# Kernel tuning notes

Hardware: AMD Instinct MI355X
Metric: run time of the kernel (lower is better)

Reference implementation:

```python
import jax, jax.numpy as jnp
import numpy as np

NUM_QUBITS = 12
ENC_COPIES = 1
ANSATZ_COPIES = 2
BATCH = 1024
NUM_THETAS = NUM_QUBITS * (ANSATZ_COPIES + 1) * 2  # 72

_H = jnp.asarray(np.array([[1.0, 1.0], [1.0, -1.0]], np.complex64) / np.sqrt(2.0))


def _apply_1q(state, U, q):
    # state: [B, 2, 2, ..., 2] (n qubit axes); apply 2x2 unitary U on qubit q
    s = jnp.moveaxis(state, 1 + q, -1)
    s = jnp.einsum('...j,ij->...i', s, U)
    return jnp.moveaxis(s, -1, 1 + q)


def _apply_zpow(state, t, q):
    # cirq Z**t = diag(1, e^{i*pi*t}); t is scalar or per-batch [B]
    n = state.ndim - 1
    phase = jnp.exp(1j * jnp.pi * t).astype(jnp.complex64)
    factor = jnp.stack([jnp.ones_like(phase), phase], axis=-1)
    if factor.ndim == 2:  # batched exponent -> broadcast over other qubit axes
        factor = factor.reshape((factor.shape[0],) + (1,) * (n - 1) + (2,))
    s = jnp.moveaxis(state, 1 + q, -1)
    return jnp.moveaxis(s * factor, -1, 1 + q)


def _ypow_unitary(t):
    # cirq Y**t up to global phase e^{i*pi*t/2} (irrelevant for Z expectations)
    a = 0.5 * jnp.pi * t
    c, s = jnp.cos(a), jnp.sin(a)
    return jnp.stack([jnp.stack([c, -s]), jnp.stack([s, c])]).astype(jnp.complex64)


def _apply_cnot(state, c, t):
    s = jnp.moveaxis(state, (1 + c, 1 + t), (-2, -1))
    s = jnp.stack([s[..., 0, :], s[..., 1, ::-1]], axis=-2)
    return jnp.moveaxis(s, (-2, -1), (1 + c, 1 + t))


def _encoding_block(state, x):
    # FirstOrderPauliZEncoding: per copy, per qubit: H then Z**x_q
    for _ in range(ENC_COPIES):
        for q in range(NUM_QUBITS):
            state = _apply_1q(state, _H, q)
            state = _apply_zpow(state, x[:, q], q)
    return state


def _ansatz_block(state, th, with_cnot):
    # EfficientSU2 layer: Y**th[q,0], Z**th[q,1] per qubit, then CNOT chain
    for q in range(NUM_QUBITS):
        state = _apply_1q(state, _ypow_unitary(th[q, 0]), q)
        state = _apply_zpow(state, th[q, 1], q)
    if with_cnot:
        for q in range(NUM_QUBITS - 1):
            state = _apply_cnot(state, q, q + 1)
    return state


_enc = jax.checkpoint(_encoding_block)
_ans_cnot = jax.checkpoint(lambda st, th: _ansatz_block(st, th, True))
_ans_last = jax.checkpoint(lambda st, th: _ansatz_block(st, th, False))


def _circuit(inputs, thetas):
    b = inputs.shape[0]
    state = jnp.zeros((b, 2 ** NUM_QUBITS), jnp.complex64).at[:, 0].set(1.0)
    state = state.reshape((b,) + (2,) * NUM_QUBITS)
    state = _enc(state, inputs)
    th = thetas.reshape(ANSATZ_COPIES + 1, NUM_QUBITS, 2)
    for l in range(ANSATZ_COPIES + 1):
        state = (_ans_cnot if l < ANSATZ_COPIES else _ans_last)(state, th[l])
    # readouts: <Z_q> for each qubit
    probs = state.real ** 2 + state.imag ** 2
    exps = []
    for q in range(NUM_QUBITS):
        axes = tuple(a for a in range(1, NUM_QUBITS + 1) if a != 1 + q)
        p = probs.sum(axis=axes)  # [B, 2]
        exps.append(p[:, 0] - p[:, 1])
    return jnp.stack(exps, axis=-1)  # [B, NUM_QUBITS]


def setup_inputs() -> dict:
    key = jax.random.key(0)
    k1, k2 = jax.random.split(key)
    inputs = jax.random.uniform(k1, (BATCH, NUM_QUBITS), jnp.float32)
    thetas = jax.random.uniform(k2, (NUM_THETAS,), jnp.float32, minval=-1.0, maxval=1.0)
    return {"inputs": inputs, "thetas": thetas}


def reference(inputs, thetas):
    return _circuit(inputs, thetas)
```

## Files before the change

kernel.cpp:

```cpp
#include <hip/hip_runtime.h>


#define PI_F 3.14159265358979323846f
#define NR 32
#define PAD 66

__device__ __forceinline__ float2 cmul(float2 a, float2 b) {
    return make_float2(a.x*b.x - a.y*b.y, a.x*b.y + a.y*b.x);
}
__device__ __forceinline__ float2 cmulc(float2 a, float2 b) {
    return make_float2(a.x*b.x + a.y*b.y, a.y*b.x - a.x*b.y);
}

template<int RB>
__device__ __forceinline__ void ypow_reg(float2 (&a)[NR], float c, float s) {
    #pragma unroll
    for (int r0 = 0; r0 < NR; ++r0) {
        if ((r0 >> RB) & 1) continue;
        const int r1 = r0 | (1 << RB);
        float2 a0 = a[r0], a1 = a[r1];
        a[r0] = make_float2(c*a0.x - s*a1.x, c*a0.y - s*a1.y);
        a[r1] = make_float2(s*a0.x + c*a1.x, s*a0.y + c*a1.y);
    }
}

__device__ __forceinline__ void exchange_AB(float2 (&a)[NR], float2* buf,
                                            int w, int lane, float c6, float s6) {
    float2* wb = buf + w * (NR * PAD);
    __syncthreads();
    #pragma unroll
    for (int r = 0; r < NR; ++r)
        wb[r * PAD + (lane & 31) * 2 + (lane >> 5)] = a[r];
    __syncthreads();
    const int g = lane >> 1;
    const float k0 = (lane & 1) ? s6 : c6;
    const float k1 = (lane & 1) ? c6 : -s6;
    #pragma unroll
    for (int r = 0; r < NR; ++r) {
        float2 p0 = wb[g * PAD + r * 2];
        float2 p1 = wb[g * PAD + r * 2 + 1];
        a[r] = make_float2(k0*p0.x + k1*p1.x, k0*p0.y + k1*p1.y);
    }
}

__device__ __forceinline__ void exchange_BA(float2 (&a)[NR], float2* buf,
                                            int w, int lane, float c0, float s0) {
    __syncthreads();
    const int p6w = lane ^ (w << 5);
    #pragma unroll
    for (int r = 0; r < NR; ++r)
        buf[p6w * PAD + r * 2 + w] = a[r];
    __syncthreads();
    const float k0 = w ? s0 : c0;
    const float k1 = w ? c0 : -s0;
    #pragma unroll
    for (int rp = 0; rp < NR; ++rp) {
        const int ylow = (rp << 6) | lane;
        const int t = ylow ^ (ylow >> 1);
        const int base = (t >> 5) * PAD + (t & 31) * 2;
        float2 p0 = buf[base];
        float2 p1 = buf[base + 1];
        a[rp] = make_float2(k0*p0.x + k1*p1.x, k0*p0.y + k1*p1.y);
    }
}

__device__ __forceinline__ void ypow_block_regA(float2 (&a)[NR], const float* __restrict__ th) {
    { float s,c; __sincosf(0.5f*PI_F*th[2],  &s,&c); ypow_reg<4>(a,c,s); }
    { float s,c; __sincosf(0.5f*PI_F*th[4],  &s,&c); ypow_reg<3>(a,c,s); }
    { float s,c; __sincosf(0.5f*PI_F*th[6],  &s,&c); ypow_reg<2>(a,c,s); }
    { float s,c; __sincosf(0.5f*PI_F*th[8],  &s,&c); ypow_reg<1>(a,c,s); }
    { float s,c; __sincosf(0.5f*PI_F*th[10], &s,&c); ypow_reg<0>(a,c,s); }
}
__device__ __forceinline__ void ypow_block_regB(float2 (&a)[NR], const float* __restrict__ th) {
    { float s,c; __sincosf(0.5f*PI_F*th[14], &s,&c); ypow_reg<4>(a,c,s); }
    { float s,c; __sincosf(0.5f*PI_F*th[16], &s,&c); ypow_reg<3>(a,c,s); }
    { float s,c; __sincosf(0.5f*PI_F*th[18], &s,&c); ypow_reg<2>(a,c,s); }
    { float s,c; __sincosf(0.5f*PI_F*th[20], &s,&c); ypow_reg<1>(a,c,s); }
    { float s,c; __sincosf(0.5f*PI_F*th[22], &s,&c); ypow_reg<0>(a,c,s); }
}

__device__ __forceinline__ void fused_z_B(float2 (&a)[NR], int w, int lane,
                                          const float* __restrict__ th) {
    float alpha = w ? th[1] : 0.0f;
    #pragma unroll
    for (int k = 0; k < 6; ++k)
        alpha += ((lane >> k) & 1) ? th[2*(6-k)+1] : 0.0f;
    float2 zb; __sincosf(PI_F * alpha, &zb.y, &zb.x);
    float2 zq[5];
    #pragma unroll
    for (int j = 0; j < 5; ++j)
        __sincosf(PI_F * th[2*(11-j)+1], &zq[j].y, &zq[j].x);
    float2 cur = zb;
    a[0] = cmul(a[0], cur);
    #pragma unroll
    for (int k = 1; k < NR; ++k) {
        const int bit = __builtin_ctz(k);
        const int g = k ^ (k >> 1);
        cur = ((g >> bit) & 1) ? cmul(cur, zq[bit]) : cmulc(cur, zq[bit]);
        a[g] = cmul(a[g], cur);
    }
}

__global__ __launch_bounds__(128) void vqc_kernel(
    const float* __restrict__ inputs,
    const float* __restrict__ thetas,
    float* __restrict__ out)
{
    __shared__ __align__(16) float2 buf[64 * PAD];
    __shared__ float redBuf[24];

    const int b = blockIdx.x;
    const int tid = threadIdx.x;
    const int w = tid >> 6;
    const int lane = tid & 63;
    const float* x = inputs + b * 12;

    float2 a[NR];

    float phb = 0.0f;
    #pragma unroll
    for (int k = 0; k < 6; ++k)
        phb += ((lane >> k) & 1) ? x[11 - k] : 0.0f;
    float2 cisb; __sincosf(PI_F * phb, &cisb.y, &cisb.x);
    float2 E;    __sincosf(PI_F * x[0], &E.y, &E.x);
    float s0, c0; __sincosf(0.5f * PI_F * thetas[0], &s0, &c0);
    float2 Fw = w ? make_float2(s0 + c0 * E.x,  c0 * E.y)
                  : make_float2(c0 - s0 * E.x, -s0 * E.y);
    float2 g0 = cmul(Fw, cisb);
    g0.x *= 0.015625f; g0.y *= 0.015625f;
    float2 zr[5];
    #pragma unroll
    for (int j = 0; j < 5; ++j)
        __sincosf(PI_F * x[5 - j], &zr[j].y, &zr[j].x);
    {
        float2 cur = g0;
        a[0] = cur;
        #pragma unroll
        for (int k = 1; k < NR; ++k) {
            const int bit = __builtin_ctz(k);
            const int g = k ^ (k >> 1);
            cur = ((g >> bit) & 1) ? cmul(cur, zr[bit]) : cmulc(cur, zr[bit]);
            a[g] = cur;
        }
    }

    const float* th0 = thetas;
    const float* th1 = thetas + 24;
    const float* th2 = thetas + 48;

    ypow_block_regA(a, th0);
    { float s,c; __sincosf(0.5f*PI_F*th0[12], &s,&c); exchange_AB(a, buf, w, lane, c, s); }
    ypow_block_regB(a, th0);
    fused_z_B(a, w, lane, th0);
    { float s,c; __sincosf(0.5f*PI_F*th1[0],  &s,&c); exchange_BA(a, buf, w, lane, c, s); }

    ypow_block_regA(a, th1);
    { float s,c; __sincosf(0.5f*PI_F*th1[12], &s,&c); exchange_AB(a, buf, w, lane, c, s); }
    ypow_block_regB(a, th1);
    fused_z_B(a, w, lane, th1);
    { float s,c; __sincosf(0.5f*PI_F*th2[0],  &s,&c); exchange_BA(a, buf, w, lane, c, s); }

    ypow_block_regA(a, th2);
    { float s,c; __sincosf(0.5f*PI_F*th2[12], &s,&c); exchange_AB(a, buf, w, lane, c, s); }
    ypow_block_regB(a, th2);

    float totalP = 0.0f;
    float D[5] = {0, 0, 0, 0, 0};
    #pragma unroll
    for (int r = 0; r < NR; ++r) {
        const float p = a[r].x * a[r].x + a[r].y * a[r].y;
        totalP += p;
        #pragma unroll
        for (int j = 0; j < 5; ++j)
            D[j] += ((r >> j) & 1) ? -p : p;
    }
    #pragma unroll
    for (int q = 0; q < 12; ++q) {
        float v;
        if (q == 0)       v = w ? -totalP : totalP;
        else if (q <= 6)  v = ((lane >> (6 - q)) & 1) ? -totalP : totalP;
        else              v = D[11 - q];
        #pragma unroll
        for (int off = 32; off >= 1; off >>= 1)
            v += __shfl_xor(v, off, 64);
        if (lane == 0) redBuf[w * 12 + q] = v;
    }
    __syncthreads();
    if (tid < 12) out[b * 12 + tid] = redBuf[tid] + redBuf[12 + tid];
}

extern "C" void kernel_launch(void* const* d_in, const int* in_sizes, int n_in,
                              void* d_out, int out_size, void* d_ws, size_t ws_size,
                              hipStream_t stream) {
    const float* inputs = (const float*)d_in[0];
    const float* thetas = (const float*)d_in[1];
    float* out = (float*)d_out;
    vqc_kernel<<<dim3(1024), dim3(128), 0, stream>>>(inputs, thetas, out);
}
```

Baseline: 78.01 us.

## Split state across four wavefronts with 16 registers each and swizzled LDS exchanges

Each batch item now runs on 256 threads (four waves) holding 16 amplitudes per thread instead of 128 threads holding 32. Two qubits move from registers to the wave index, so the exchanges and the encoding, Z-phase and readout logic are rewritten to apply paired 2x2 rotations through XOR-swizzled 32 KB shared buffers read as float4. The exchange after the first ansatz layer drops its leading barrier and relies on an s_waitcnt instead. The goal is lower register pressure and more parallelism per item, at the cost of more shared memory per block and more LDS traffic per amplitude.

New measurement: 146.7 us. 1.88x slower.

```diff
diff --git a/kernel.cpp b/kernel.cpp
--- a/kernel.cpp
+++ b/kernel.cpp
@@ -2,8 +2,7 @@
 
 
 #define PI_F 3.14159265358979323846f
-#define NR 32
-#define PAD 66
+#define NR 16
 
 __device__ __forceinline__ float2 cmul(float2 a, float2 b) {
     return make_float2(a.x*b.x - a.y*b.y, a.x*b.y + a.y*b.x);
@@ -24,71 +23,88 @@
     }
 }
 
-__device__ __forceinline__ void exchange_AB(float2 (&a)[NR], float2* buf,
-                                            int w, int lane, float c6, float s6) {
-    float2* wb = buf + w * (NR * PAD);
-    __syncthreads();
-    #pragma unroll
-    for (int r = 0; r < NR; ++r)
-        wb[r * PAD + (lane & 31) * 2 + (lane >> 5)] = a[r];
-    __syncthreads();
-    const int g = lane >> 1;
-    const float k0 = (lane & 1) ? s6 : c6;
-    const float k1 = (lane & 1) ? c6 : -s6;
-    #pragma unroll
-    for (int r = 0; r < NR; ++r) {
-        float2 p0 = wb[g * PAD + r * 2];
-        float2 p1 = wb[g * PAD + r * 2 + 1];
-        a[r] = make_float2(k0*p0.x + k1*p1.x, k0*p0.y + k1*p1.y);
-    }
-}
-
-__device__ __forceinline__ void exchange_BA(float2 (&a)[NR], float2* buf,
-                                            int w, int lane, float c0, float s0) {
-    __syncthreads();
-    const int p6w = lane ^ (w << 5);
-    #pragma unroll
-    for (int r = 0; r < NR; ++r)
-        buf[p6w * PAD + r * 2 + w] = a[r];
-    __syncthreads();
-    const float k0 = w ? s0 : c0;
-    const float k1 = w ? c0 : -s0;
-    #pragma unroll
-    for (int rp = 0; rp < NR; ++rp) {
-        const int ylow = (rp << 6) | lane;
-        const int t = ylow ^ (ylow >> 1);
-        const int base = (t >> 5) * PAD + (t & 31) * 2;
-        float2 p0 = buf[base];
-        float2 p1 = buf[base + 1];
-        a[rp] = make_float2(k0*p0.x + k1*p1.x, k0*p0.y + k1*p1.y);
-    }
-}
-
-__device__ __forceinline__ void ypow_block_regA(float2 (&a)[NR], const float* __restrict__ th) {
-    { float s,c; __sincosf(0.5f*PI_F*th[2],  &s,&c); ypow_reg<4>(a,c,s); }
+__device__ __forceinline__ void ypowA(float2 (&a)[NR], const float* __restrict__ th) {
     { float s,c; __sincosf(0.5f*PI_F*th[4],  &s,&c); ypow_reg<3>(a,c,s); }
     { float s,c; __sincosf(0.5f*PI_F*th[6],  &s,&c); ypow_reg<2>(a,c,s); }
     { float s,c; __sincosf(0.5f*PI_F*th[8],  &s,&c); ypow_reg<1>(a,c,s); }
     { float s,c; __sincosf(0.5f*PI_F*th[10], &s,&c); ypow_reg<0>(a,c,s); }
 }
-__device__ __forceinline__ void ypow_block_regB(float2 (&a)[NR], const float* __restrict__ th) {
-    { float s,c; __sincosf(0.5f*PI_F*th[14], &s,&c); ypow_reg<4>(a,c,s); }
+__device__ __forceinline__ void ypowB(float2 (&a)[NR], const float* __restrict__ th) {
     { float s,c; __sincosf(0.5f*PI_F*th[16], &s,&c); ypow_reg<3>(a,c,s); }
     { float s,c; __sincosf(0.5f*PI_F*th[18], &s,&c); ypow_reg<2>(a,c,s); }
     { float s,c; __sincosf(0.5f*PI_F*th[20], &s,&c); ypow_reg<1>(a,c,s); }
     { float s,c; __sincosf(0.5f*PI_F*th[22], &s,&c); ypow_reg<0>(a,c,s); }
 }
 
+template<bool PRE_SYNC>
+__device__ __forceinline__ void exchange_AB(float2 (&a)[NR], char* bufc,
+                                            int w, int lane,
+                                            float c6, float s6, float c7, float s7) {
+    if (PRE_SYNC) __syncthreads();
+    const int wbyte = (w << 13) | ((lane & 15) << 5) | ((lane >> 4) << 3);
+    #pragma unroll
+    for (int r = 0; r < NR; ++r)
+        *(float2*)(bufc + ((wbyte | (r << 9)) ^ ((r & 7) << 4))) = a[r];
+    asm volatile("s_waitcnt lgkmcnt(0)" ::: "memory");
+    const int g = lane >> 2;
+    const float y60 = (lane & 2) ? s6 : c6;
+    const float y61 = (lane & 2) ? c6 : -s6;
+    const float y70 = (lane & 1) ? s7 : c7;
+    const float y71 = (lane & 1) ? c7 : -s7;
+    const float k00 = y60*y70, k01 = y60*y71, k10 = y61*y70, k11 = y61*y71;
+    const int rbyte = (w << 13) | (g << 9);
+    const int kx = (g & 7) << 4;
+    #pragma unroll
+    for (int R = 0; R < NR; ++R) {
+        const int base = rbyte | (R << 5);
+        float4 p01 = *(const float4*)(bufc + (base ^ kx));
+        float4 p23 = *(const float4*)(bufc + ((base | 16) ^ kx));
+        a[R] = make_float2(k00*p01.x + k01*p01.z + k10*p23.x + k11*p23.z,
+                           k00*p01.y + k01*p01.w + k10*p23.y + k11*p23.w);
+    }
+}
+
+__device__ __forceinline__ void exchange_BA(float2 (&a)[NR], char* bufc,
+                                            int w, int lane,
+                                            float c0, float s0, float c1, float s1) {
+    __syncthreads();
+    const int v_  = (w >> 1) & 1;
+    const int u_  = v_ ^ (w & 1);
+    const int l5u = (lane >> 5) ^ u_;
+    const int wbyte = (l5u << 14) | ((lane & 31) << 9) | (u_ << 4) | (v_ << 3);
+    const int wkx = (lane & 7) << 4;
+    #pragma unroll
+    for (int R = 0; R < NR; ++R)
+        *(float2*)(bufc + ((wbyte | (R << 5)) ^ wkx)) = a[R];
+    __syncthreads();
+    const float ky00 = (w & 2) ? s0 : c0;
+    const float ky01 = (w & 2) ? c0 : -s0;
+    const float ky10 = (w & 1) ? s1 : c1;
+    const float ky11 = (w & 1) ? c1 : -s1;
+    const float k00 = ky10*ky00, k01 = ky10*ky01, k10 = ky11*ky00, k11 = ky11*ky01;
+    #pragma unroll
+    for (int r = 0; r < NR; ++r) {
+        const int ylow = (r << 6) | lane;
+        const int t = ylow ^ (ylow >> 1);
+        const int base = t << 5;
+        const int kx = t & 0x70;
+        float4 p01 = *(const float4*)(bufc + (base ^ kx));
+        float4 p23 = *(const float4*)(bufc + ((base | 16) ^ kx));
+        a[r] = make_float2(k00*p01.x + k01*p01.z + k10*p23.x + k11*p23.z,
+                           k00*p01.y + k01*p01.w + k10*p23.y + k11*p23.w);
+    }
+}
+
 __device__ __forceinline__ void fused_z_B(float2 (&a)[NR], int w, int lane,
                                           const float* __restrict__ th) {
-    float alpha = w ? th[1] : 0.0f;
+    float alpha = ((w & 2) ? th[1] : 0.0f) + ((w & 1) ? th[3] : 0.0f);
     #pragma unroll
     for (int k = 0; k < 6; ++k)
-        alpha += ((lane >> k) & 1) ? th[2*(6-k)+1] : 0.0f;
+        alpha += ((lane >> k) & 1) ? th[2*(7-k)+1] : 0.0f;
     float2 zb; __sincosf(PI_F * alpha, &zb.y, &zb.x);
-    float2 zq[5];
-    #pragma unroll
-    for (int j = 0; j < 5; ++j)
+    float2 zq[4];
+    #pragma unroll
+    for (int j = 0; j < 4; ++j)
         __sincosf(PI_F * th[2*(11-j)+1], &zq[j].y, &zq[j].x);
     float2 cur = zb;
     a[0] = cmul(a[0], cur);
@@ -101,13 +117,13 @@
     }
 }
 
-__global__ __launch_bounds__(128) void vqc_kernel(
+__global__ __launch_bounds__(256, 4) void vqc_kernel(
     const float* __restrict__ inputs,
     const float* __restrict__ thetas,
     float* __restrict__ out)
 {
-    __shared__ __align__(16) float2 buf[64 * PAD];
-    __shared__ float redBuf[24];
+    __shared__ __align__(16) char bufc[32768];
+    __shared__ float redBuf[48];
 
     const int b = blockIdx.x;
     const int tid = threadIdx.x;
@@ -122,15 +138,19 @@
     for (int k = 0; k < 6; ++k)
         phb += ((lane >> k) & 1) ? x[11 - k] : 0.0f;
     float2 cisb; __sincosf(PI_F * phb, &cisb.y, &cisb.x);
-    float2 E;    __sincosf(PI_F * x[0], &E.y, &E.x);
-    float s0, c0; __sincosf(0.5f * PI_F * thetas[0], &s0, &c0);
-    float2 Fw = w ? make_float2(s0 + c0 * E.x,  c0 * E.y)
-                  : make_float2(c0 - s0 * E.x, -s0 * E.y);
-    float2 g0 = cmul(Fw, cisb);
+    float2 E0; __sincosf(PI_F * x[0], &E0.y, &E0.x);
+    float2 E1; __sincosf(PI_F * x[1], &E1.y, &E1.x);
+    float sa, ca; __sincosf(0.5f * PI_F * thetas[0], &sa, &ca);
+    float sb, cb; __sincosf(0.5f * PI_F * thetas[2], &sb, &cb);
+    float2 F0 = (w & 2) ? make_float2(sa + ca*E0.x,  ca*E0.y)
+                        : make_float2(ca - sa*E0.x, -sa*E0.y);
+    float2 F1 = (w & 1) ? make_float2(sb + cb*E1.x,  cb*E1.y)
+                        : make_float2(cb - sb*E1.x, -sb*E1.y);
+    float2 g0 = cmul(cmul(F0, F1), cisb);
     g0.x *= 0.015625f; g0.y *= 0.015625f;
-    float2 zr[5];
-    #pragma unroll
-    for (int j = 0; j < 5; ++j)
+    float2 zr[4];
+    #pragma unroll
+    for (int j = 0; j < 4; ++j)
         __sincosf(PI_F * x[5 - j], &zr[j].y, &zr[j].x);
     {
         float2 cur = g0;
@@ -148,45 +168,63 @@
     const float* th1 = thetas + 24;
     const float* th2 = thetas + 48;
 
-    ypow_block_regA(a, th0);
-    { float s,c; __sincosf(0.5f*PI_F*th0[12], &s,&c); exchange_AB(a, buf, w, lane, c, s); }
-    ypow_block_regB(a, th0);
+    ypowA(a, th0);
+    { float s6,c6,s7,c7;
+      __sincosf(0.5f*PI_F*th0[12], &s6,&c6);
+      __sincosf(0.5f*PI_F*th0[14], &s7,&c7);
+      exchange_AB<false>(a, bufc, w, lane, c6,s6,c7,s7); }
+    ypowB(a, th0);
     fused_z_B(a, w, lane, th0);
-    { float s,c; __sincosf(0.5f*PI_F*th1[0],  &s,&c); exchange_BA(a, buf, w, lane, c, s); }
-
-    ypow_block_regA(a, th1);
-    { float s,c; __sincosf(0.5f*PI_F*th1[12], &s,&c); exchange_AB(a, buf, w, lane, c, s); }
-    ypow_block_regB(a, th1);
+    { float s0,c0,s1,c1;
+      __sincosf(0.5f*PI_F*th1[0], &s0,&c0);
+      __sincosf(0.5f*PI_F*th1[2], &s1,&c1);
+      exchange_BA(a, bufc, w, lane, c0,s0,c1,s1); }
+
+    ypowA(a, th1);
+    { float s6,c6,s7,c7;
+      __sincosf(0.5f*PI_F*th1[12], &s6,&c6);
+      __sincosf(0.5f*PI_F*th1[14], &s7,&c7);
+      exchange_AB<true>(a, bufc, w, lane, c6,s6,c7,s7); }
+    ypowB(a, th1);
     fused_z_B(a, w, lane, th1);
-    { float s,c; __sincosf(0.5f*PI_F*th2[0],  &s,&c); exchange_BA(a, buf, w, lane, c, s); }
-
-    ypow_block_regA(a, th2);
-    { float s,c; __sincosf(0.5f*PI_F*th2[12], &s,&c); exchange_AB(a, buf, w, lane, c, s); }
-    ypow_block_regB(a, th2);
+    { float s0,c0,s1,c1;
+      __sincosf(0.5f*PI_F*th2[0], &s0,&c0);
+      __sincosf(0.5f*PI_F*th2[2], &s1,&c1);
+      exchange_BA(a, bufc, w, lane, c0,s0,c1,s1); }
+
+    ypowA(a, th2);
+    { float s6,c6,s7,c7;
+      __sincosf(0.5f*PI_F*th2[12], &s6,&c6);
+      __sincosf(0.5f*PI_F*th2[14], &s7,&c7);
+      exchange_AB<true>(a, bufc, w, lane, c6,s6,c7,s7); }
+    ypowB(a, th2);
 
     float totalP = 0.0f;
-    float D[5] = {0, 0, 0, 0, 0};
+    float D[4] = {0, 0, 0, 0};
     #pragma unroll
     for (int r = 0; r < NR; ++r) {
         const float p = a[r].x * a[r].x + a[r].y * a[r].y;
         totalP += p;
         #pragma unroll
-        for (int j = 0; j < 5; ++j)
+        for (int j = 0; j < 4; ++j)
             D[j] += ((r >> j) & 1) ? -p : p;
     }
     #pragma unroll
     for (int q = 0; q < 12; ++q) {
         float v;
-        if (q == 0)       v = w ? -totalP : totalP;
-        else if (q <= 6)  v = ((lane >> (6 - q)) & 1) ? -totalP : totalP;
-        else              v = D[11 - q];
+        if (q == 0)      v = (w & 2) ? -totalP : totalP;
+        else if (q == 1) v = (w & 1) ? -totalP : totalP;
+        else if (q <= 7) v = ((lane >> (7 - q)) & 1) ? -totalP : totalP;
+        else             v = D[11 - q];
         #pragma unroll
         for (int off = 32; off >= 1; off >>= 1)
             v += __shfl_xor(v, off, 64);
         if (lane == 0) redBuf[w * 12 + q] = v;
     }
     __syncthreads();
-    if (tid < 12) out[b * 12 + tid] = redBuf[tid] + redBuf[12 + tid];
+    if (tid < 12)
+        out[b * 12 + tid] = redBuf[tid] + redBuf[12 + tid]
+                          + redBuf[24 + tid] + redBuf[36 + tid];
 }
 
 extern "C" void kernel_launch(void* const* d_in, const int* in_sizes, int n_in,
@@ -195,5 +233,5 @@
     const float* inputs = (const float*)d_in[0];
     const float* thetas = (const float*)d_in[1];
     float* out = (float*)d_out;
-    vqc_kernel<<<dim3(1024), dim3(128), 0, stream>>>(inputs, thetas, out);
-}
+    vqc_kernel<<<dim3(1024), dim3(256), 0, stream>>>(inputs, thetas, out);
+}
```
